# Performance work log

Hardware: AMD Instinct MI355X
Metric: run time of the kernel (lower is better)

## Reference

```python
import jax, jax.numpy as jnp
import numpy as np

HEADS = 8
KEY_DIM = 64
VALUE_DIM = 64


def setup_inputs() -> dict:
    key = jax.random.key(0)
    ks = jax.random.split(key, 6)
    B, I, O, T, S = 2, 512, 512, 2048, 2048
    E = KEY_DIM * HEADS  # 512
    Ev = VALUE_DIM * HEADS  # 512
    return {
        "x": jax.random.normal(ks[0], (B, I, T), dtype=jnp.float32),
        "y": jax.random.normal(ks[1], (B, O, S), dtype=jnp.float32),
        "mask": jnp.zeros((T, S), dtype=jnp.float32),
        "Wk": jax.random.normal(ks[2], (E, I), dtype=jnp.float32) * (I ** -0.5),
        "Wv": jax.random.normal(ks[3], (Ev, I), dtype=jnp.float32) * (I ** -0.5),
        "Wq": jax.random.normal(ks[4], (E, O), dtype=jnp.float32) * (O ** -0.5),
        "W": jax.random.normal(ks[5], (O, Ev), dtype=jnp.float32) * (Ev ** -0.5),
        "b": jnp.zeros((O,), dtype=jnp.float32),
    }


def reference(x, y, mask, Wk, Wv, Wq, W, b):
    B, I, T = x.shape
    S = y.shape[2]
    H, dk, dv = HEADS, KEY_DIM, VALUE_DIM
    scaling = dk ** -0.5
    # 1x1 Conv1d projections == channel GEMMs; reshape (B, H*d, L) -> (B*H, d, L)
    keys = jnp.einsum('ei,bit->bet', Wk, x).reshape(B * H, dk, T)
    values = jnp.einsum('ei,bit->bet', Wv, x).reshape(B * H, dv, T)
    queries = jnp.einsum('eo,bos->bes', Wq, y).reshape(B * H, dk, S)
    # scores: [B*H, T, S]
    dot = jnp.einsum('bkt,bks->bts', keys, queries)
    dot = dot + mask[None, :, :]
    # torch Softmax(1) on [bh, T, S] normalizes over T (keys axis);
    # note: scaling applied AFTER mask add, as in the original.
    attention = jax.nn.softmax(scaling * dot, axis=1)
    # weighted values: [B*H, dv, S] -> [B, H*dv, S]
    output = jnp.einsum('bvt,bts->bvs', values, attention).reshape(B, H * dv, S)
    # final Linear over channel dim applied to (B, S, H*dv)
    return jnp.einsum('bvs,ov->bso', output, W) + b
```

## Files before the change

### kernel.cpp

```cpp
#include <hip/hip_runtime.h>
#include <stdint.h>

typedef unsigned short u16;
typedef unsigned int u32;

#define B_    2
#define DK    64
#define T_    2048
#define S_    2048
#define CI    512
#define CO    512
#define E_    512

typedef short  short8 __attribute__((ext_vector_type(8)));
typedef __bf16 bf16x8 __attribute__((ext_vector_type(8)));
typedef float  f32x4  __attribute__((ext_vector_type(4)));

static __device__ __forceinline__ u16 f2bf(float f) {
    return __builtin_bit_cast(u16, (__bf16)f);
}

static __device__ __forceinline__ float bf2f(u16 h) {
    return __uint_as_float((u32)h << 16);
}

static __device__ __forceinline__ short8 ld8(const u16* p) {
    return *(const short8*)p;
}

static __device__ __forceinline__ f32x4 mfma_bf16(short8 a, short8 b, f32x4 c) {
    return __builtin_amdgcn_mfma_f32_16x16x32_bf16(
        __builtin_bit_cast(bf16x8, a), __builtin_bit_cast(bf16x8, b), c, 0, 0, 0);
}

__global__ __launch_bounds__(256) void k_prep(const float* __restrict__ x, const float* __restrict__ y,
                                              const float* __restrict__ wk, const float* __restrict__ wv,
                                              const float* __restrict__ wq, const float* __restrict__ wf,
                                              const float* __restrict__ mask,
                                              u16* __restrict__ xt, u16* __restrict__ yt,
                                              u16* __restrict__ wkb, u16* __restrict__ wvb,
                                              u16* __restrict__ wqb, u16* __restrict__ wfb,
                                              u16* __restrict__ mt) {
    __shared__ float tile[32][33];
    int bid = blockIdx.x;
    if (bid < 4096) {
        int bx = bid & 63, by = (bid >> 6) & 15, bz = bid >> 10;
        int tsel = bz >> 1, b = bz & 1;
        const float* src = tsel ? y : x;
        u16* dst = tsel ? yt : xt;
        int t0 = bx * 32, i0 = by * 32;
        int tx = threadIdx.x & 31, ty = threadIdx.x >> 5;
#pragma unroll
        for (int r = 0; r < 4; r++)
            tile[ty + r * 8][tx] = src[(size_t)(b * CI + i0 + ty + r * 8) * T_ + t0 + tx];
        __syncthreads();
#pragma unroll
        for (int r = 0; r < 4; r++)
            dst[(size_t)(b * T_ + t0 + ty + r * 8) * CI + i0 + tx] = f2bf(tile[tx][ty + r * 8]);
    } else if (bid < 4608) {
        int off = ((bid - 4096) * 256 + threadIdx.x) * 8;
        int w = off >> 18, r = off & 262143;
        const float* s = (w == 0) ? wk : (w == 1) ? wv : (w == 2) ? wq : wf;
        u16* d = (w == 0) ? wkb : (w == 1) ? wvb : (w == 2) ? wqb : wfb;
        float4 a0 = *(const float4*)(s + r);
        float4 a1 = *(const float4*)(s + r + 4);
        short8 o;
        o[0] = f2bf(a0.x); o[1] = f2bf(a0.y); o[2] = f2bf(a0.z); o[3] = f2bf(a0.w);
        o[4] = f2bf(a1.x); o[5] = f2bf(a1.y); o[6] = f2bf(a1.z); o[7] = f2bf(a1.w);
        *(short8*)(d + r) = o;
    } else {
        int mb = bid - 4608;
        int t0 = (mb & 63) * 32, s0 = (mb >> 6) * 32;
        int tx = threadIdx.x & 31, ty = threadIdx.x >> 5;
        const float msc = 0.125f * 1.44269504088896f;
#pragma unroll
        for (int r = 0; r < 4; r++)
            tile[ty + r * 8][tx] = mask[(size_t)(t0 + ty + r * 8) * S_ + s0 + tx];
        __syncthreads();
#pragma unroll
        for (int r = 0; r < 4; r++)
            mt[(size_t)(s0 + ty + r * 8) * T_ + t0 + tx] = f2bf(tile[tx][ty + r * 8] * msc);
    }
}

__global__ __launch_bounds__(256) void k_proj3(const u16* __restrict__ xt, const u16* __restrict__ yt,
                                               const u16* __restrict__ wkb, const u16* __restrict__ wvb,
                                               const u16* __restrict__ wqb,
                                               u16* __restrict__ ktd, u16* __restrict__ vtd,
                                               u16* __restrict__ qtd, int p_base) {
    int bi = blockIdx.x;
    int p = p_base + (bi >> 8);
    int r = bi & 255;
    int et = r & 3, tt = r >> 2;
    int wv = threadIdx.x >> 6, lane = threadIdx.x & 63;
    int col = lane & 15, q = lane >> 4;
    int b = tt >> 5;
    int t0 = (tt & 31) * 64 + (wv >> 1) * 32;
    int e0 = et * 128 + (wv & 1) * 64;
    const u16* src = (p == 0) ? yt : xt;
    const u16* wb  = (p == 0) ? wqb : (p == 1) ? wkb : wvb;
    const u16* ap0 = src + (size_t)(b * T_ + t0 + col) * CI + q * 8;
    const u16* bp0 = wb + (size_t)(e0 + col) * CI + q * 8;
    f32x4 acc[2][4] = {};
#pragma unroll 4
    for (int ks = 0; ks < 16; ks++) {
        short8 a0 = ld8(ap0 + ks * 32);
        short8 a1 = ld8(ap0 + 16 * CI + ks * 32);
#pragma unroll
        for (int nt = 0; nt < 4; nt++) {
            short8 bb = ld8(bp0 + (size_t)(nt * 16) * CI + ks * 32);
            acc[0][nt] = mfma_bf16(a0, bb, acc[0][nt]);
            acc[1][nt] = mfma_bf16(a1, bb, acc[1][nt]);
        }
    }
    u16* dst = (p == 0) ? qtd : (p == 1) ? ktd : vtd;
    if (p < 2) {
#pragma unroll
        for (int mt = 0; mt < 2; mt++)
#pragma unroll
            for (int nt = 0; nt < 4; nt++) {
                int e = e0 + nt * 16 + col, h = e >> 6, k = e & 63;
                u16* dp = dst + ((size_t)(b * 8 + h) * T_ + t0 + mt * 16 + q * 4) * DK + k;
                dp[0] = f2bf(acc[mt][nt][0]);
                dp[DK] = f2bf(acc[mt][nt][1]);
                dp[2 * DK] = f2bf(acc[mt][nt][2]);
                dp[3 * DK] = f2bf(acc[mt][nt][3]);
            }
    } else {
#pragma unroll
        for (int mt = 0; mt < 2; mt++)
#pragma unroll
            for (int nt = 0; nt < 4; nt++) {
                int e = e0 + nt * 16 + col, h = e >> 6, v = e & 63;
                uint2 pk;
                pk.x = f2bf(acc[mt][nt][0]) | ((u32)f2bf(acc[mt][nt][1]) << 16);
                pk.y = f2bf(acc[mt][nt][2]) | ((u32)f2bf(acc[mt][nt][3]) << 16);
                *(uint2*)(dst + ((size_t)(b * 8 + h) * DK + v) * T_ + t0 + mt * 16 + q * 4) = pk;
            }
    }
}


#define ATTN_ITER(T0, KC, MC4, MCF, KN, MN4, MNF, TN)  do {                         \
    short8 vb0 = ld8(vbase + (T0));                                                 \
    short8 vb1 = ld8(vbase + 16 * (size_t)T_ + (T0));                               \
    short8 vb2 = ld8(vbase + 32 * (size_t)T_ + (T0));                               \
    short8 vb3 = ld8(vbase + 48 * (size_t)T_ + (T0));                               \
    f32x4 s0g[4], s1g[4];                                                           \
    _Pragma("unroll") for (int g = 0; g < 4; g++) {                                 \
        f32x4 z = {};                                                               \
        s0g[g] = mfma_bf16(KC[0], qa[g][0], z);                                     \
        s0g[g] = mfma_bf16(KC[1], qa[g][1], s0g[g]);                                \
        s1g[g] = mfma_bf16(KC[2], qa[g][0], z);                                     \
        s1g[g] = mfma_bf16(KC[3], qa[g][1], s1g[g]);                                \
    }                                                                               \
    KN[0] = ld8(kbase + (size_t)(TN) * DK);                                         \
    KN[1] = ld8(kbase + (size_t)(TN) * DK + 32);                                    \
    KN[2] = ld8(kbase + (size_t)((TN) + 4) * DK);                                   \
    KN[3] = ld8(kbase + (size_t)((TN) + 4) * DK + 32);                              \
    if constexpr (MODE == 1) {                                                      \
        _Pragma("unroll") for (int g = 0; g < 4; g++) {                             \
            MN4[g][0] = *(const ushort4*)(mtb[g] + (TN));                           \
            MN4[g][1] = *(const ushort4*)(mtb[g] + (TN) + 4);                       \
        }                                                                           \
    } else {                                                                        \
        _Pragma("unroll") for (int g = 0; g < 4; g++)                               \
        _Pragma("unroll") for (int st = 0; st < 2; st++)                            \
        _Pragma("unroll") for (int rr = 0; rr < 4; rr++)                            \
            MNF[g][st * 4 + rr] =                                                   \
                mbs[g][(size_t)((TN) + q * 8 + st * 4 + rr) * S_] * sc;             \
    }                                                                               \
    _Pragma("unroll") for (int g = 0; g < 4; g++) {                                 \
        bf16x8 pbv;                                                                 \
        float lsum = 0.f;                                                           \
        _Pragma("unroll") for (int i = 0; i < 8; i++) {                             \
            float sv = (i < 4) ? s0g[g][i & 3] : s1g[g][i & 3];                     \
            float mv;                                                               \
            if constexpr (MODE == 1)                                                \
                mv = bf2f(((const u16*)&MC4[g][i >> 2])[i & 3]);                    \
            else                                                                    \
                mv = MCF[g][i];                                                     \
            float p = __builtin_amdgcn_exp2f(fmaf(sv, sc, mv));                     \
            lsum += p;                                                              \
            pbv[i] = (__bf16)p;                                                     \
        }                                                                           \
        l_part[g] += lsum;                                                          \
        short8 pa = __builtin_bit_cast(short8, pbv);                                \
        oacc[g][0] = mfma_bf16(vb0, pa, oacc[g][0]);                                \
        oacc[g][1] = mfma_bf16(vb1, pa, oacc[g][1]);                                \
        oacc[g][2] = mfma_bf16(vb2, pa, oacc[g][2]);                                \
        oacc[g][3] = mfma_bf16(vb3, pa, oacc[g][3]);                                \
    }                                                                               \
} while (0)

template<int MODE>
__global__ __launch_bounds__(512, 2) void k_attn(const u16* __restrict__ kt, const u16* __restrict__ qt,
                                                 const u16* __restrict__ vt, const float* __restrict__ mask,
                                                 const u16* __restrict__ mt, u16* __restrict__ oa) {
    __shared__ struct { float O[8][16][68]; float L[8][16]; } Sm;
    int wv = threadIdx.x >> 6, lane = threadIdx.x & 63;
    int col = lane & 15, q = lane >> 4;
    int bid = blockIdx.x;
    int j = bid >> 3;
    int bh = (bid & 7) * 2 + (j >> 5);
    int s_base = (j & 31) * 64;
    int sg = s_base + col;
    const int t_begin = wv * (T_ / 8);
    const int t_end = t_begin + (T_ / 8);
    short8 qa[4][2];
#pragma unroll
    for (int g = 0; g < 4; g++) {
        const u16* qp = qt + (size_t)(bh * S_ + sg + g * 16) * DK + q * 8;
        qa[g][0] = ld8(qp);
        qa[g][1] = ld8(qp + 32);
    }
    int tperm = ((col >> 2) << 3) | (col & 3);
    const u16* kbase = kt + (size_t)bh * T_ * DK + (size_t)tperm * DK + q * 8;
    const u16* vbase = vt + (size_t)bh * DK * T_ + (size_t)col * T_ + q * 8;
    const float* mbs[4];
    const u16* mtb[4];
#pragma unroll
    for (int g = 0; g < 4; g++) {
        mbs[g] = mask + sg + g * 16;
        mtb[g] = mt + (size_t)(sg + g * 16) * T_ + q * 8;
    }
    float l_part[4] = {0.f, 0.f, 0.f, 0.f};
    f32x4 oacc[4][4] = {};
    const float sc = 0.125f * 1.44269504088896f;

    short8 kA[4], kB[4];
    ushort4 mA4[4][2], mB4[4][2];
    float mAf[4][8], mBf[4][8];
    kA[0] = ld8(kbase + (size_t)t_begin * DK);
    kA[1] = ld8(kbase + (size_t)t_begin * DK + 32);
    kA[2] = ld8(kbase + (size_t)(t_begin + 4) * DK);
    kA[3] = ld8(kbase + (size_t)(t_begin + 4) * DK + 32);
    if constexpr (MODE == 1) {
#pragma unroll
        for (int g = 0; g < 4; g++) {
            mA4[g][0] = *(const ushort4*)(mtb[g] + t_begin);
            mA4[g][1] = *(const ushort4*)(mtb[g] + t_begin + 4);
        }
    } else {
#pragma unroll
        for (int g = 0; g < 4; g++)
#pragma unroll
            for (int st = 0; st < 2; st++)
#pragma unroll
                for (int rr = 0; rr < 4; rr++)
                    mAf[g][st * 4 + rr] =
                        mbs[g][(size_t)(t_begin + q * 8 + st * 4 + rr) * S_] * sc;
    }

    for (int t0 = t_begin; t0 < t_end; t0 += 64) {
        ATTN_ITER(t0, kA, mA4, mAf, kB, mB4, mBf, t0 + 32);
        int tn2 = (t0 + 64 < t_end) ? (t0 + 64) : t_begin;
        ATTN_ITER(t0 + 32, kB, mB4, mBf, kA, mA4, mAf, tn2);
    }

#pragma unroll
    for (int g = 0; g < 4; g++) {
        float lr = l_part[g];
        lr += __shfl_xor(lr, 16);
        lr += __shfl_xor(lr, 32);
        l_part[g] = lr;
    }

    int b = bh >> 3, h = bh & 7;
    __syncthreads();
#pragma unroll
    for (int g = 0; g < 4; g++) {
#pragma unroll
        for (int nt = 0; nt < 4; nt++)
            *(f32x4*)&Sm.O[wv][col][nt * 16 + q * 4] = oacc[g][nt];
        if (lane < 16)
            Sm.L[wv][lane] = l_part[g];
        __syncthreads();
#pragma unroll
        for (int e = 0; e < 2; e++) {
            int f = (int)threadIdx.x + e * 512;
            int s = f >> 6, v = f & 63;
            float acc = 0.f, lt = 0.f;
#pragma unroll
            for (int c = 0; c < 8; c++) {
                acc += Sm.O[c][s][v];
                lt += Sm.L[c][s];
            }
            oa[(size_t)(b * S_ + s_base + g * 16 + s) * E_ + h * DK + v] = f2bf(acc / lt);
        }
        __syncthreads();
    }
}

__global__ __launch_bounds__(256) void k_final(const u16* __restrict__ oa, const u16* __restrict__ wfb,
                                               const float* __restrict__ bias, float* __restrict__ out) {
    int bi = blockIdx.x;
    int et = bi & 7, tt = bi >> 3;
    int wv = threadIdx.x >> 6, lane = threadIdx.x & 63;
    int col = lane & 15, q = lane >> 4;
    int b = tt >> 5;
    int s0 = (tt & 31) * 64 + (wv >> 1) * 32;
    int o0 = et * 64 + (wv & 1) * 32;
    const u16* ap0 = oa + (size_t)(b * S_ + s0 + col) * E_ + q * 8;
    const u16* bp0 = wfb + (size_t)(o0 + col) * E_ + q * 8;
    f32x4 acc[2][2] = {};
#pragma unroll 4
    for (int ks = 0; ks < 16; ks++) {
        short8 a0 = ld8(ap0 + ks * 32);
        short8 a1 = ld8(ap0 + 16 * E_ + ks * 32);
#pragma unroll
        for (int nt = 0; nt < 2; nt++) {
            short8 bb = ld8(bp0 + (size_t)(nt * 16) * E_ + ks * 32);
            acc[0][nt] = mfma_bf16(a0, bb, acc[0][nt]);
            acc[1][nt] = mfma_bf16(a1, bb, acc[1][nt]);
        }
    }
#pragma unroll
    for (int mt = 0; mt < 2; mt++)
#pragma unroll
        for (int nt = 0; nt < 2; nt++) {
            int o = o0 + nt * 16 + col;
            float bn = bias[o];
#pragma unroll
            for (int r = 0; r < 4; r++) {
                int s = s0 + mt * 16 + q * 4 + r;
                out[(size_t)(b * S_ + s) * CO + o] = acc[mt][nt][r] + bn;
            }
        }
}

extern "C" void kernel_launch(void* const* d_in, const int* in_sizes, int n_in,
                              void* d_out, int out_size, void* d_ws, size_t ws_size,
                              hipStream_t stream) {
    const float* x    = (const float*)d_in[0];
    const float* y    = (const float*)d_in[1];
    const float* mask = (const float*)d_in[2];
    const float* Wk   = (const float*)d_in[3];
    const float* Wv   = (const float*)d_in[4];
    const float* Wq   = (const float*)d_in[5];
    const float* Wf   = (const float*)d_in[6];
    const float* bias = (const float*)d_in[7];
    float* out = (float*)d_out;

    u16* ws = (u16*)d_ws;
    u16* XT  = ws;
    u16* YT  = XT + 2097152;
    u16* WKB = YT + 2097152;
    u16* WVB = WKB + 262144;
    u16* WQB = WVB + 262144;
    u16* WFB = WQB + 262144;
    u16* KT  = WFB + 262144;
    u16* QT  = KT + 2097152;
    u16* MT  = QT + 2097152;
    u16* VTs = MT + 4194304;
    u16* OA  = XT;

    int use_mt = (ws_size >= (size_t)27262976) ? 1 : 0;
    int has_vt = (ws_size >= (size_t)31457280) ? 1 : 0;
    u16* VT = has_vt ? VTs : YT;

    k_prep<<<use_mt ? 8704 : 4608, 256, 0, stream>>>(x, y, Wk, Wv, Wq, Wf, mask,
                                                     XT, YT, WKB, WVB, WQB, WFB, MT);
    if (has_vt) {
        k_proj3<<<768, 256, 0, stream>>>(XT, YT, WKB, WVB, WQB, KT, VT, QT, 0);
    } else {
        k_proj3<<<512, 256, 0, stream>>>(XT, YT, WKB, WVB, WQB, KT, VT, QT, 0);
        k_proj3<<<256, 256, 0, stream>>>(XT, YT, WKB, WVB, WQB, KT, VT, QT, 2);
    }
    if (use_mt)
        k_attn<1><<<512, 512, 0, stream>>>(KT, QT, VT, mask, MT, OA);
    else
        k_attn<0><<<512, 512, 0, stream>>>(KT, QT, VT, mask, MT, OA);
    k_final<<<512, 256, 0, stream>>>(OA, WFB, bias, out);
}
```

Before: 208.1 us.

## Software-pipeline global loads in projection, attention and final GEMM loops

The projection and final GEMM loops are fully unrolled and prefetch the next k-step's A/B fragments into registers while the current MFMAs run. The attention loop now double-buffers V fragments alongside K, loading the next tile's V one iteration early. MFMA blocks are also wrapped in s_setprio raises. This targets global-load latency exposed before each MFMA, at the cost of extra VGPRs that could lower occupancy.

```diff
diff --git a/kernel.cpp b/kernel.cpp
--- a/kernel.cpp
+++ b/kernel.cpp
@@ -102,15 +102,26 @@
     const u16* ap0 = src + (size_t)(b * T_ + t0 + col) * CI + q * 8;
     const u16* bp0 = wb + (size_t)(e0 + col) * CI + q * 8;
     f32x4 acc[2][4] = {};
-#pragma unroll 4
+    short8 a0 = ld8(ap0), a1 = ld8(ap0 + 16 * CI);
+    short8 b0 = ld8(bp0), b1 = ld8(bp0 + 16 * CI);
+    short8 b2 = ld8(bp0 + 32 * CI), b3 = ld8(bp0 + 48 * CI);
+#pragma unroll
     for (int ks = 0; ks < 16; ks++) {
-        short8 a0 = ld8(ap0 + ks * 32);
-        short8 a1 = ld8(ap0 + 16 * CI + ks * 32);
-#pragma unroll
-        for (int nt = 0; nt < 4; nt++) {
-            short8 bb = ld8(bp0 + (size_t)(nt * 16) * CI + ks * 32);
-            acc[0][nt] = mfma_bf16(a0, bb, acc[0][nt]);
-            acc[1][nt] = mfma_bf16(a1, bb, acc[1][nt]);
+        short8 na0, na1, nb0, nb1, nb2, nb3;
+        if (ks < 15) {
+            na0 = ld8(ap0 + (ks + 1) * 32);
+            na1 = ld8(ap0 + 16 * CI + (ks + 1) * 32);
+            nb0 = ld8(bp0 + (ks + 1) * 32);
+            nb1 = ld8(bp0 + 16 * CI + (ks + 1) * 32);
+            nb2 = ld8(bp0 + 32 * CI + (ks + 1) * 32);
+            nb3 = ld8(bp0 + 48 * CI + (ks + 1) * 32);
+        }
+        acc[0][0] = mfma_bf16(a0, b0, acc[0][0]); acc[1][0] = mfma_bf16(a1, b0, acc[1][0]);
+        acc[0][1] = mfma_bf16(a0, b1, acc[0][1]); acc[1][1] = mfma_bf16(a1, b1, acc[1][1]);
+        acc[0][2] = mfma_bf16(a0, b2, acc[0][2]); acc[1][2] = mfma_bf16(a1, b2, acc[1][2]);
+        acc[0][3] = mfma_bf16(a0, b3, acc[0][3]); acc[1][3] = mfma_bf16(a1, b3, acc[1][3]);
+        if (ks < 15) {
+            a0 = na0; a1 = na1; b0 = nb0; b1 = nb1; b2 = nb2; b3 = nb3;
         }
     }
     u16* dst = (p == 0) ? qtd : (p == 1) ? ktd : vtd;
@@ -141,12 +152,9 @@
 }
 
 
-#define ATTN_ITER(T0, KC, MC4, MCF, KN, MN4, MNF, TN)  do {                         \
-    short8 vb0 = ld8(vbase + (T0));                                                 \
-    short8 vb1 = ld8(vbase + 16 * (size_t)T_ + (T0));                               \
-    short8 vb2 = ld8(vbase + 32 * (size_t)T_ + (T0));                               \
-    short8 vb3 = ld8(vbase + 48 * (size_t)T_ + (T0));                               \
+#define ATTN_ITER(KC, VC, MC4, MCF, KN, VN, MN4, MNF, TN)  do {                     \
     f32x4 s0g[4], s1g[4];                                                           \
+    __builtin_amdgcn_s_setprio(1);                                                  \
     _Pragma("unroll") for (int g = 0; g < 4; g++) {                                 \
         f32x4 z = {};                                                               \
         s0g[g] = mfma_bf16(KC[0], qa[g][0], z);                                     \
@@ -154,10 +162,15 @@
         s1g[g] = mfma_bf16(KC[2], qa[g][0], z);                                     \
         s1g[g] = mfma_bf16(KC[3], qa[g][1], s1g[g]);                                \
     }                                                                               \
+    __builtin_amdgcn_s_setprio(0);                                                  \
     KN[0] = ld8(kbase + (size_t)(TN) * DK);                                         \
     KN[1] = ld8(kbase + (size_t)(TN) * DK + 32);                                    \
     KN[2] = ld8(kbase + (size_t)((TN) + 4) * DK);                                   \
     KN[3] = ld8(kbase + (size_t)((TN) + 4) * DK + 32);                              \
+    VN[0] = ld8(vbase + (TN));                                                      \
+    VN[1] = ld8(vbase + 16 * (size_t)T_ + (TN));                                    \
+    VN[2] = ld8(vbase + 32 * (size_t)T_ + (TN));                                    \
+    VN[3] = ld8(vbase + 48 * (size_t)T_ + (TN));                                    \
     if constexpr (MODE == 1) {                                                      \
         _Pragma("unroll") for (int g = 0; g < 4; g++) {                             \
             MN4[g][0] = *(const ushort4*)(mtb[g] + (TN));                           \
@@ -186,10 +199,12 @@
         }                                                                           \
         l_part[g] += lsum;                                                          \
         short8 pa = __builtin_bit_cast(short8, pbv);                                \
-        oacc[g][0] = mfma_bf16(vb0, pa, oacc[g][0]);                                \
-        oacc[g][1] = mfma_bf16(vb1, pa, oacc[g][1]);                                \
-        oacc[g][2] = mfma_bf16(vb2, pa, oacc[g][2]);                                \
-        oacc[g][3] = mfma_bf16(vb3, pa, oacc[g][3]);                                \
+        __builtin_amdgcn_s_setprio(1);                                              \
+        oacc[g][0] = mfma_bf16(VC[0], pa, oacc[g][0]);                              \
+        oacc[g][1] = mfma_bf16(VC[1], pa, oacc[g][1]);                              \
+        oacc[g][2] = mfma_bf16(VC[2], pa, oacc[g][2]);                              \
+        oacc[g][3] = mfma_bf16(VC[3], pa, oacc[g][3]);                              \
+        __builtin_amdgcn_s_setprio(0);                                              \
     }                                                                               \
 } while (0)
 
@@ -228,13 +243,17 @@
     f32x4 oacc[4][4] = {};
     const float sc = 0.125f * 1.44269504088896f;
 
-    short8 kA[4], kB[4];
+    short8 kA[4], kB[4], vA[4], vB[4];
     ushort4 mA4[4][2], mB4[4][2];
     float mAf[4][8], mBf[4][8];
     kA[0] = ld8(kbase + (size_t)t_begin * DK);
     kA[1] = ld8(kbase + (size_t)t_begin * DK + 32);
     kA[2] = ld8(kbase + (size_t)(t_begin + 4) * DK);
     kA[3] = ld8(kbase + (size_t)(t_begin + 4) * DK + 32);
+    vA[0] = ld8(vbase + t_begin);
+    vA[1] = ld8(vbase + 16 * (size_t)T_ + t_begin);
+    vA[2] = ld8(vbase + 32 * (size_t)T_ + t_begin);
+    vA[3] = ld8(vbase + 48 * (size_t)T_ + t_begin);
     if constexpr (MODE == 1) {
 #pragma unroll
         for (int g = 0; g < 4; g++) {
@@ -253,9 +272,9 @@
     }
 
     for (int t0 = t_begin; t0 < t_end; t0 += 64) {
-        ATTN_ITER(t0, kA, mA4, mAf, kB, mB4, mBf, t0 + 32);
+        ATTN_ITER(kA, vA, mA4, mAf, kB, vB, mB4, mBf, t0 + 32);
         int tn2 = (t0 + 64 < t_end) ? (t0 + 64) : t_begin;
-        ATTN_ITER(t0 + 32, kB, mB4, mBf, kA, mA4, mAf, tn2);
+        ATTN_ITER(kB, vB, mB4, mBf, kA, vA, mA4, mAf, tn2);
     }
 
 #pragma unroll
@@ -304,15 +323,21 @@
     const u16* ap0 = oa + (size_t)(b * S_ + s0 + col) * E_ + q * 8;
     const u16* bp0 = wfb + (size_t)(o0 + col) * E_ + q * 8;
     f32x4 acc[2][2] = {};
-#pragma unroll 4
+    short8 a0 = ld8(ap0), a1 = ld8(ap0 + 16 * E_);
+    short8 b0 = ld8(bp0), b1 = ld8(bp0 + 16 * E_);
+#pragma unroll
     for (int ks = 0; ks < 16; ks++) {
-        short8 a0 = ld8(ap0 + ks * 32);
-        short8 a1 = ld8(ap0 + 16 * E_ + ks * 32);
-#pragma unroll
-        for (int nt = 0; nt < 2; nt++) {
-            short8 bb = ld8(bp0 + (size_t)(nt * 16) * E_ + ks * 32);
-            acc[0][nt] = mfma_bf16(a0, bb, acc[0][nt]);
-            acc[1][nt] = mfma_bf16(a1, bb, acc[1][nt]);
+        short8 na0, na1, nb0, nb1;
+        if (ks < 15) {
+            na0 = ld8(ap0 + (ks + 1) * 32);
+            na1 = ld8(ap0 + 16 * E_ + (ks + 1) * 32);
+            nb0 = ld8(bp0 + (ks + 1) * 32);
+            nb1 = ld8(bp0 + 16 * E_ + (ks + 1) * 32);
+        }
+        acc[0][0] = mfma_bf16(a0, b0, acc[0][0]); acc[1][0] = mfma_bf16(a1, b0, acc[1][0]);
+        acc[0][1] = mfma_bf16(a0, b1, acc[0][1]); acc[1][1] = mfma_bf16(a1, b1, acc[1][1]);
+        if (ks < 15) {
+            a0 = na0; a1 = na1; b0 = nb0; b1 = nb1;
         }
     }
 #pragma unroll
```

After: 252.7 us. +21.4%, slower.
